# Kernel tuning notes

Hardware: AMD Instinct MI355X
Metric: run time of the kernel (lower is better)

Reference implementation:

```python
import jax, jax.numpy as jnp
import numpy as np

N = 8192          # number of atoms
N_ELEM = 95       # r2r4 table size (elements 0..94)
EPS = 1e-12


def setup_inputs() -> dict:
    key = jax.random.key(0)
    k1, k2, k3 = jax.random.split(key, 3)
    atomic_numbers = jax.random.randint(k1, (N,), 0, N_ELEM)
    # positions in a ~60 Angstrom box so pair distances are realistic
    positions = jax.random.uniform(k2, (N, 3), dtype=jnp.float32) * 60.0
    r2r4 = jax.random.uniform(k3, (N_ELEM,), dtype=jnp.float32)
    # Becke-Johnson damping parameters (PBE D3-BJ)
    a1 = jnp.float32(0.4289)
    a2 = jnp.float32(4.4407)
    s6 = jnp.float32(1.0)
    s8 = jnp.float32(0.7875)
    return {"atomic_numbers": atomic_numbers, "positions": positions,
            "r2r4": r2r4, "a1": a1, "a2": a2, "s6": s6, "s8": s8}


def reference(atomic_numbers, positions, r2r4, a1, a2, s6, s8):
    # Per-atom-type gather (present in source; mathematically unused because
    # the source hard-codes c6 = c8 = 1 via all-ones LazyTensors).
    r2r4_z = r2r4[atomic_numbers]                      # (N,)

    # All-pairs squared distances. d appears only as d^6 and d^8, which are
    # polynomials in d2, so no sqrt is needed (also keeps diagonal smooth).
    diff = positions[:, None, :] - positions[None, :, :]   # (N, N, 3)
    d2 = jnp.sum(diff * diff, axis=-1)                     # (N, N)
    d6 = d2 * d2 * d2
    d8 = d6 * d2

    # c6 = c8 = 1  =>  tmp = a1 * sqrt(c8/c6) + a2 = a1 + a2
    tmp = a1 + a2
    tmp2 = tmp * tmp
    tmp6 = tmp2 * tmp2 * tmp2
    tmp8 = tmp6 * tmp2

    c6 = jnp.float32(1.0)
    c8 = jnp.float32(1.0)
    D_ij = -s6 * c6 / (d6 + tmp6 + EPS) - s8 * c8 / (d8 + tmp8 + EPS)

    # mask d > eps  <=>  d2 > eps^2 (removes self-terms)
    mask = d2 > EPS * EPS
    D_ij = jnp.where(mask, D_ij, jnp.float32(0.0))

    # a_i = sum_j D_ij ; energy = sum_i a_i
    return jnp.sum(D_ij) + jnp.float32(0.0) * jnp.sum(r2r4_z)
```

## Files before the change

kernel.cpp:

```cpp
#include <hip/hip_runtime.h>

#define NA 8192
#define IT 128
#define JT 64
#define NI (NA / IT)
#define NJOB 4160
#define WPB 4
#define BLOCK (WPB * 64)
#define NBLK (NJOB / WPB)
#define S_OF(I) ((I) * (129 - (I)))

typedef float v2f __attribute__((ext_vector_type(2)));

__device__ __forceinline__ float bcast(float v, int k) {
    return __int_as_float(__builtin_amdgcn_readlane(__float_as_int(v), k));
}

__global__ __launch_bounds__(BLOCK, 6) void dftd3_pair_energy(
    const float* __restrict__ pos,
    const float* __restrict__ p_a1, const float* __restrict__ p_a2,
    const float* __restrict__ p_s6, const float* __restrict__ p_s8,
    float* __restrict__ partial, int* __restrict__ cnt,
    float* __restrict__ out)
{
    const int tid  = threadIdx.x;
    const int lane = tid & 63;
    const int w = __builtin_amdgcn_readfirstlane(blockIdx.x * WPB + (tid >> 6));

    int I = (int)((129.0f - sqrtf(16641.0f - 4.0f * (float)w)) * 0.5f);
    if (I < 0) I = 0;
    if (I > NI - 1) I = NI - 1;
    while (S_OF(I + 1) <= w) ++I;
    while (S_OF(I) > w) --I;
    const int J = 2 * I + (w - S_OF(I));
    const bool edge = (w - S_OF(I)) < 2;

    const float PS = 0.015625f;
    const int j = J * JT + lane;
    const float vxj = pos[3 * j + 0] * PS;
    const float vyj = pos[3 * j + 1] * PS;
    const float vzj = pos[3 * j + 2] * PS;

    const int i0 = I * IT + 2 * lane;
    const v2f xi = { pos[3 * i0 + 0] * PS, pos[3 * i0 + 3] * PS };
    const v2f yi = { pos[3 * i0 + 1] * PS, pos[3 * i0 + 4] * PS };
    const v2f zi = { pos[3 * i0 + 2] * PS, pos[3 * i0 + 5] * PS };

    const float a1 = p_a1[0], a2 = p_a2[0];
    const float s6 = p_s6[0], s8 = p_s8[0];
    const float tmp  = a1 + a2;
    const float tmp2 = tmp * tmp;
    const float tmp6 = tmp2 * tmp2 * tmp2;
    const float tmp8 = tmp6 * tmp2;
    const float T6s = (tmp6 + 1e-12f) * 1.4551915e-11f;
    const float T8s = (tmp8 + 1e-12f) * 3.5527137e-15f;
    const float c6 = -2.0f * s6 * 1.4551915e-11f;
    const float c8 = -2.0f * s8 * 3.5527137e-15f;

    float accx = 0.0f, accy = 0.0f;

    auto body = [&](int k, bool masked) {
        float sx = bcast(vxj, k);
        float sy = bcast(vyj, k);
        float sz = bcast(vzj, k);
        v2f dx = xi - sx;
        v2f dy = yi - sy;
        v2f dz = zi - sz;
        v2f d2 = __builtin_elementwise_fma(dx, dx,
                 __builtin_elementwise_fma(dy, dy, dz * dz));
        v2f d4 = d2 * d2;
        v2f A  = __builtin_elementwise_fma(d4, d2, (v2f)T6s);
        v2f B  = __builtin_elementwise_fma(d4, d4, (v2f)T8s);
        v2f num = __builtin_elementwise_fma((v2f)c6, B, (v2f)c8 * A);
        v2f den = A * B;
        float t = den.x * den.y;
        float r = __builtin_amdgcn_rcpf(t);
        float numx = num.x, numy = num.y;
        if (masked) {
            const int jk = J * JT + k;
            numx = (jk > i0)     ? numx : 0.0f;
            numy = (jk > i0 + 1) ? numy : 0.0f;
        }
        accx = fmaf(numx, den.y * r, accx);
        accy = fmaf(numy, den.x * r, accy);
    };

    if (edge) {
        #pragma unroll 8
        for (int k = 0; k < JT; ++k) body(k, true);
    } else {
        #pragma unroll 8
        for (int k = 0; k < JT; ++k) body(k, false);
    }

    float acc = accx + accy;

    #pragma unroll
    for (int off = 32; off > 0; off >>= 1)
        acc += __shfl_xor(acc, off, 64);

    __shared__ float wsum[WPB];
    __shared__ int lastflag;
    if (lane == 0) wsum[tid >> 6] = acc;
    __syncthreads();
    if (tid == 0) {
        float s = 0.0f;
        #pragma unroll
        for (int q = 0; q < WPB; ++q) s += wsum[q];
        atomicExch(&partial[blockIdx.x], s);
        __threadfence();
        int old = atomicAdd(cnt, 1);
        lastflag = (old == NBLK - 1);
    }
    __syncthreads();
    if (lastflag) {
        __threadfence();
        float s = 0.0f;
        for (int t = tid; t < NBLK; t += BLOCK)
            s += atomicAdd(&partial[t], 0.0f);
        #pragma unroll
        for (int off = 32; off > 0; off >>= 1)
            s += __shfl_xor(s, off, 64);
        if (lane == 0) wsum[tid >> 6] = s;
        __syncthreads();
        if (tid == 0) {
            float tot = 0.0f;
            #pragma unroll
            for (int q = 0; q < WPB; ++q) tot += wsum[q];
            out[0] = tot;
        }
    }
}

extern "C" void kernel_launch(void* const* d_in, const int* in_sizes, int n_in,
                              void* d_out, int out_size, void* d_ws, size_t ws_size,
                              hipStream_t stream) {
    const float* pos = (const float*)d_in[1];
    const float* a1  = (const float*)d_in[3];
    const float* a2  = (const float*)d_in[4];
    const float* s6  = (const float*)d_in[5];
    const float* s8  = (const float*)d_in[6];
    float* partial = (float*)d_ws;
    int*   cnt     = (int*)((char*)d_ws + 65536);
    float* out     = (float*)d_out;

    hipMemsetAsync(cnt, 0, sizeof(int), stream);

    dftd3_pair_energy<<<dim3(NBLK), BLOCK, 0, stream>>>(pos, a1, a2, s6, s8,
                                                        partial, cnt, out);
}
```

Before: 88.46 us.

## Interleave four independent pair chains per step and reduce via strided atomic slots

The inner loop now processes four j-columns (stride 16) per iteration with separate accumulators, exposing more independent work to hide FMA and rcp latency. Blocks grow to 8 waves with a lower occupancy hint. The final reduction replaces per-block partial stores with atomicAdd into 64 padded slots that the last block reads, and the memset now also zeroes those slots. This adds register pressure and atomic contention, and makes the summation order nondeterministic.

```diff
diff --git a/kernel.cpp b/kernel.cpp
--- a/kernel.cpp
+++ b/kernel.cpp
@@ -5,9 +5,12 @@
 #define JT 64
 #define NI (NA / IT)
 #define NJOB 4160
-#define WPB 4
+#define WPB 8
 #define BLOCK (WPB * 64)
 #define NBLK (NJOB / WPB)
+#define NSLOT 64
+#define SLOT_STRIDE 16
+#define NCH 4
 #define S_OF(I) ((I) * (129 - (I)))
 
 typedef float v2f __attribute__((ext_vector_type(2)));
@@ -16,11 +19,11 @@
     return __int_as_float(__builtin_amdgcn_readlane(__float_as_int(v), k));
 }
 
-__global__ __launch_bounds__(BLOCK, 6) void dftd3_pair_energy(
+__global__ __launch_bounds__(BLOCK, 4) void dftd3_pair_energy(
     const float* __restrict__ pos,
     const float* __restrict__ p_a1, const float* __restrict__ p_a2,
     const float* __restrict__ p_s6, const float* __restrict__ p_s8,
-    float* __restrict__ partial, int* __restrict__ cnt,
+    float* __restrict__ slots, int* __restrict__ cnt,
     float* __restrict__ out)
 {
     const int tid  = threadIdx.x;
@@ -57,57 +60,82 @@
     const float c6 = -2.0f * s6 * 1.4551915e-11f;
     const float c8 = -2.0f * s8 * 3.5527137e-15f;
 
-    float accx = 0.0f, accy = 0.0f;
+    v2f acc[NCH];
+    #pragma unroll
+    for (int c = 0; c < NCH; ++c) acc[c] = (v2f){0.0f, 0.0f};
 
-    auto body = [&](int k, bool masked) {
-        float sx = bcast(vxj, k);
-        float sy = bcast(vyj, k);
-        float sz = bcast(vzj, k);
-        v2f dx = xi - sx;
-        v2f dy = yi - sy;
-        v2f dz = zi - sz;
-        v2f d2 = __builtin_elementwise_fma(dx, dx,
-                 __builtin_elementwise_fma(dy, dy, dz * dz));
-        v2f d4 = d2 * d2;
-        v2f A  = __builtin_elementwise_fma(d4, d2, (v2f)T6s);
-        v2f B  = __builtin_elementwise_fma(d4, d4, (v2f)T8s);
-        v2f num = __builtin_elementwise_fma((v2f)c6, B, (v2f)c8 * A);
-        v2f den = A * B;
-        float t = den.x * den.y;
-        float r = __builtin_amdgcn_rcpf(t);
-        float numx = num.x, numy = num.y;
+    auto quad = [&](int k, bool masked) {
+        v2f dx[NCH], dy[NCH], dz[NCH], d2[NCH], d4[NCH];
+        v2f A[NCH], B[NCH], num[NCH], den[NCH];
+        float r[NCH];
+        #pragma unroll
+        for (int c = 0; c < NCH; ++c) {
+            const int kc = k + 16 * c;
+            float sx = bcast(vxj, kc);
+            float sy = bcast(vyj, kc);
+            float sz = bcast(vzj, kc);
+            dx[c] = xi - sx;
+            dy[c] = yi - sy;
+            dz[c] = zi - sz;
+        }
+        #pragma unroll
+        for (int c = 0; c < NCH; ++c) {
+            d2[c] = __builtin_elementwise_fma(dx[c], dx[c],
+                    __builtin_elementwise_fma(dy[c], dy[c], dz[c] * dz[c]));
+            d4[c] = d2[c] * d2[c];
+        }
+        #pragma unroll
+        for (int c = 0; c < NCH; ++c) {
+            A[c] = __builtin_elementwise_fma(d4[c], d2[c], (v2f)T6s);
+            B[c] = __builtin_elementwise_fma(d4[c], d4[c], (v2f)T8s);
+        }
+        #pragma unroll
+        for (int c = 0; c < NCH; ++c) {
+            num[c] = __builtin_elementwise_fma((v2f)c6, B[c], (v2f)c8 * A[c]);
+            den[c] = A[c] * B[c];
+        }
+        #pragma unroll
+        for (int c = 0; c < NCH; ++c)
+            r[c] = __builtin_amdgcn_rcpf(den[c].x * den[c].y);
         if (masked) {
-            const int jk = J * JT + k;
-            numx = (jk > i0)     ? numx : 0.0f;
-            numy = (jk > i0 + 1) ? numy : 0.0f;
+            #pragma unroll
+            for (int c = 0; c < NCH; ++c) {
+                const int jk = J * JT + k + 16 * c;
+                num[c].x = (jk > i0)     ? num[c].x : 0.0f;
+                num[c].y = (jk > i0 + 1) ? num[c].y : 0.0f;
+            }
         }
-        accx = fmaf(numx, den.y * r, accx);
-        accy = fmaf(numy, den.x * r, accy);
+        #pragma unroll
+        for (int c = 0; c < NCH; ++c) {
+            v2f inv = { den[c].y * r[c], den[c].x * r[c] };
+            acc[c] = __builtin_elementwise_fma(num[c], inv, acc[c]);
+        }
     };
 
     if (edge) {
-        #pragma unroll 8
-        for (int k = 0; k < JT; ++k) body(k, true);
+        #pragma unroll 2
+        for (int k = 0; k < JT / NCH; ++k) quad(k, true);
     } else {
-        #pragma unroll 8
-        for (int k = 0; k < JT; ++k) body(k, false);
+        #pragma unroll 2
+        for (int k = 0; k < JT / NCH; ++k) quad(k, false);
     }
 
-    float acc = accx + accy;
+    v2f accv = (acc[0] + acc[1]) + (acc[2] + acc[3]);
+    float acc_s = accv.x + accv.y;
 
     #pragma unroll
     for (int off = 32; off > 0; off >>= 1)
-        acc += __shfl_xor(acc, off, 64);
+        acc_s += __shfl_xor(acc_s, off, 64);
 
     __shared__ float wsum[WPB];
     __shared__ int lastflag;
-    if (lane == 0) wsum[tid >> 6] = acc;
+    if (lane == 0) wsum[tid >> 6] = acc_s;
     __syncthreads();
     if (tid == 0) {
         float s = 0.0f;
         #pragma unroll
         for (int q = 0; q < WPB; ++q) s += wsum[q];
-        atomicExch(&partial[blockIdx.x], s);
+        atomicAdd(&slots[(blockIdx.x & (NSLOT - 1)) * SLOT_STRIDE], s);
         __threadfence();
         int old = atomicAdd(cnt, 1);
         lastflag = (old == NBLK - 1);
@@ -116,19 +144,15 @@
     if (lastflag) {
         __threadfence();
         float s = 0.0f;
-        for (int t = tid; t < NBLK; t += BLOCK)
-            s += atomicAdd(&partial[t], 0.0f);
+        if (tid < NSLOT)
+            s = __hip_atomic_load(&slots[tid * SLOT_STRIDE],
+                                  __ATOMIC_ACQUIRE, __HIP_MEMORY_SCOPE_AGENT);
         #pragma unroll
         for (int off = 32; off > 0; off >>= 1)
             s += __shfl_xor(s, off, 64);
         if (lane == 0) wsum[tid >> 6] = s;
         __syncthreads();
-        if (tid == 0) {
-            float tot = 0.0f;
-            #pragma unroll
-            for (int q = 0; q < WPB; ++q) tot += wsum[q];
-            out[0] = tot;
-        }
+        if (tid == 0) out[0] = wsum[0];
     }
 }
 
@@ -140,12 +164,12 @@
     const float* a2  = (const float*)d_in[4];
     const float* s6  = (const float*)d_in[5];
     const float* s8  = (const float*)d_in[6];
-    float* partial = (float*)d_ws;
-    int*   cnt     = (int*)((char*)d_ws + 65536);
-    float* out     = (float*)d_out;
+    float* slots = (float*)d_ws;
+    int*   cnt   = (int*)((char*)d_ws + NSLOT * SLOT_STRIDE * sizeof(float));
+    float* out   = (float*)d_out;
 
-    hipMemsetAsync(cnt, 0, sizeof(int), stream);
+    hipMemsetAsync(d_ws, 0, NSLOT * SLOT_STRIDE * sizeof(float) + sizeof(int), stream);
 
     dftd3_pair_energy<<<dim3(NBLK), BLOCK, 0, stream>>>(pos, a1, a2, s6, s8,
-                                                        partial, cnt, out);
+                                                        slots, cnt, out);
 }
```

Measured after the change: 91.05 us. 1.03x slower.
